# Optimization experiments

Hardware: AMD Instinct MI355X
Metric: run time of the kernel (lower is better)

Reference implementation:

```python
import jax, jax.numpy as jnp
import numpy as np

N = 50000      # nodes
E = 800000     # edges
T = 3          # npass
ED = 64        # embedding_dim
NS = 23        # nshifts (arange(0.8, 3.0+1e-5, 0.1))
MD = NS + ED   # message_dim = 87
H = 200        # hidden width (hardcoded in module)
NMOL = 2048    # number of molecules (segments for final scatter)
RD = ED * (T + 1)  # readout input dim = 256
EPS = 1e-5

SHIFTS = jnp.asarray(np.arange(0.8, 3.0 + 1e-5, 0.1, dtype=np.float32))  # [23]


def setup_inputs() -> dict:
    key = jax.random.key(0)
    ks = jax.random.split(key, 32)
    inp = {
        'z_i': jax.random.randint(ks[0], (N,), 0, 10),
        'edge_index': jax.random.randint(ks[1], (2, E), 0, N),
        'dist_ij': jax.random.uniform(ks[2], (E, 1), dtype=jnp.float32) * 2.2 + 0.8,
        'mol_ind': jnp.sort(jax.random.randint(ks[3], (N,), 0, NMOL)),
        'emb': jax.random.normal(ks[4], (10, ED), dtype=jnp.float32),
        # per-pass update MLP params, stacked over T
        'up_bn_g': jnp.ones((T, MD), jnp.float32),
        'up_bn_b': jnp.zeros((T, MD), jnp.float32),
        'up_w1': jax.random.normal(ks[5], (T, MD, H), jnp.float32) * 0.05,
        'up_b1': jnp.zeros((T, H), jnp.float32),
        'up_w2': jax.random.normal(ks[6], (T, H, H), jnp.float32) * 0.05,
        'up_b2': jnp.zeros((T, H), jnp.float32),
        'up_w3': jax.random.normal(ks[7], (T, H, H), jnp.float32) * 0.05,
        'up_b3': jnp.zeros((T, H), jnp.float32),
        'up_w4': jax.random.normal(ks[8], (T, H, ED), jnp.float32) * 0.05,
        'up_b4': jnp.zeros((T, ED), jnp.float32),
        # readout MLP params
        'ro_bn_g': jnp.ones((RD,), jnp.float32),
        'ro_bn_b': jnp.zeros((RD,), jnp.float32),
        'ro_w1': jax.random.normal(ks[9], (RD, H), jnp.float32) * 0.05,
        'ro_b1': jnp.zeros((H,), jnp.float32),
        'ro_w2': jax.random.normal(ks[10], (H, H), jnp.float32) * 0.05,
        'ro_b2': jnp.zeros((H,), jnp.float32),
        'ro_w3': jax.random.normal(ks[11], (H, H), jnp.float32) * 0.05,
        'ro_b3': jnp.zeros((H,), jnp.float32),
        'ro_w4': jax.random.normal(ks[12], (H, 1), jnp.float32) * 0.05,
        'ro_b4': jnp.zeros((1,), jnp.float32),  # bias filled to 0 in __init__
    }
    return inp


def batchnorm(x, g, b):
    # BatchNorm1d in training mode: batch statistics, biased variance
    mu = jnp.mean(x, axis=0)
    var = jnp.mean(jnp.square(x - mu), axis=0)
    return (x - mu) * jax.lax.rsqrt(var + EPS) * g + b


def mlp(x, g, b, w1, b1, w2, b2, w3, b3, w4, b4):
    x = batchnorm(x, g, b)
    x = jax.nn.relu(x @ w1 + b1)
    x = jax.nn.relu(x @ w2 + b2)
    x = jax.nn.relu(x @ w3 + b3)
    return x @ w4 + b4


def reference(z_i, edge_index, dist_ij, mol_ind, emb,
              up_bn_g, up_bn_b, up_w1, up_b1, up_w2, up_b2, up_w3, up_b3, up_w4, up_b4,
              ro_bn_g, ro_bn_b, ro_w1, ro_b1, ro_w2, ro_b2, ro_w3, ro_b3, ro_w4, ro_b4):
    e_source, e_sink = edge_index[0], edge_index[1]
    rbf_ij = jnp.exp(-jnp.square(dist_ij - SHIFTS[None, :]))  # [E, NS]
    x_i = emb[z_i]                                            # [N, ED]
    x_list = [x_i]
    for t in range(T):
        m_ij = jnp.concatenate([rbf_ij, x_i[e_sink]], axis=1)  # [E, MD] gather
        m_i = jax.ops.segment_sum(m_ij, e_source, num_segments=N)  # scatter-sum
        x_i = x_i + 0.1 * mlp(m_i, up_bn_g[t], up_bn_b[t],
                              up_w1[t], up_b1[t], up_w2[t], up_b2[t],
                              up_w3[t], up_b3[t], up_w4[t], up_b4[t])
        x_list.append(x_i)
    x_all = jnp.concatenate(x_list, axis=1)  # [N, RD]
    y_i = mlp(x_all, ro_bn_g, ro_bn_b, ro_w1, ro_b1, ro_w2, ro_b2, ro_w3, ro_b3, ro_w4, ro_b4)
    y = jax.ops.segment_sum(y_i, mol_ind, num_segments=NMOL)  # [NMOL, 1]
    return y
```

## Files before the change

kernel.cpp:

```cpp
#include <hip/hip_runtime.h>
#include <hip/hip_bf16.h>
#include <type_traits>

#define NN 50000
#define NP 50048
#define EE 800000
#define TT 3
#define ED 64
#define NS 23
#define MD 87
#define HH 200
#define NMOL 2048
#define RD 256

#define SW 232
#define NPB2 512
#define SNB ((NN + 255) / 256)

typedef __attribute__((ext_vector_type(8))) short short8b;
typedef __attribute__((ext_vector_type(4))) float f32x4;

template <int V> using ic = std::integral_constant<int, V>;

__device__ __forceinline__ unsigned short f2bf(float f) {
  unsigned u = __float_as_uint(f);
  return (unsigned short)((u + 0x7fffu + ((u >> 16) & 1u)) >> 16);
}
__device__ __forceinline__ float ubf2f(unsigned short h) {
  return __uint_as_float(((unsigned)h) << 16);
}
__device__ __forceinline__ float bfp2f(unsigned p) {
  return __uint_as_float(p << 16) + __uint_as_float(p & 0xffff0000u);
}
__device__ __forceinline__ unsigned packsplit(float v) {
  unsigned short h = f2bf(v);
  unsigned short l = f2bf(v - ubf2f(h));
  return (unsigned)h | ((unsigned)l << 16);
}

__device__ __forceinline__ void gl2lds16(const short* g, short* l) {
  __builtin_amdgcn_global_load_lds(
      (const __attribute__((address_space(1))) unsigned int*)g,
      (__attribute__((address_space(3))) unsigned int*)l, 16, 0, 0);
}

struct WD { const float* src; short* dst; int K, N, Kpad, Npad, T; };
struct WDs { WD d[5]; };

__global__ __launch_bounds__(256) void wprep_kernel(WDs W) {
  WD w = W.d[blockIdx.y];
  int KB = w.Kpad >> 5, NT = w.Npad >> 4;
  int per = w.Npad * w.Kpad;
  int total = w.T * per;
  for (int idx = blockIdx.x * 256 + threadIdx.x; idx < total; idx += gridDim.x * 256) {
    int t = idx / per;
    int r = idx - t * per;
    int e = r & 7, lane = (r >> 3) & 63;
    int blk = r >> 9;
    int kb = blk % KB, tile = blk / KB;
    int ln = lane & 15, quad = lane >> 4;
    int n = tile * 16 + ln, k = kb * 32 + quad * 8 + e;
    float v = 0.f;
    if (k < w.K && n < w.N) v = w.src[((size_t)t * w.K + k) * w.N + n];
    unsigned short h = f2bf(v);
    unsigned short l = f2bf(v - ubf2f(h));
    size_t base = ((size_t)(t * NT + tile) * KB + kb) * 1024;
    w.dst[base + lane * 8 + e] = (short)h;
    w.dst[base + 512 + lane * 8 + e] = (short)l;
  }
}

__global__ __launch_bounds__(256) void wscale_kernel(const float* __restrict__ wsrc,
                                                     const float* __restrict__ na,
                                                     const float* __restrict__ nb,
                                                     const float* __restrict__ bsrc,
                                                     int K, int Kpad,
                                                     short* __restrict__ wsp,
                                                     float* __restrict__ bc) {
  int n = blockIdx.x;
  int k = threadIdx.x;
  int KB = Kpad >> 5;
  int tile = n >> 4, ln = n & 15;
  float contrib = 0.f;
  if (k < Kpad) {
    float v = 0.f;
    if (n < HH && k < K) {
      float w = wsrc[(size_t)k * HH + n];
      v = na[k] * w;
      contrib = nb[k] * w;
    }
    unsigned short h = f2bf(v);
    unsigned short l = f2bf(v - ubf2f(h));
    int kb = k >> 5, quad = (k & 31) >> 3, e = k & 7;
    int lane = quad * 16 + ln;
    size_t base = ((size_t)tile * KB + kb) * 1024;
    wsp[base + lane * 8 + e] = (short)h;
    wsp[base + 512 + lane * 8 + e] = (short)l;
  }
  __shared__ float sh[256];
  sh[k] = contrib;
  __syncthreads();
  for (int off = 128; off > 0; off >>= 1) {
    if (k < off) sh[k] += sh[k + off];
    __syncthreads();
  }
  if (k == 0) bc[n] = (n < HH ? bsrc[n] : 0.f) + sh[0];
}

__global__ __launch_bounds__(256) void emb_kernel(const int* __restrict__ z,
                                                  const float* __restrict__ emb,
                                                  unsigned* __restrict__ xp,
                                                  short* __restrict__ xq,
                                                  short* __restrict__ xqs) {
  int idx = blockIdx.x * 256 + threadIdx.x;
  if (idx >= NN * ED) return;
  int i = idx >> 6, d = idx & 63;
  unsigned pk = packsplit(emb[z[i] * ED + d]);
  xp[(size_t)i * RD + d] = pk;
  short h = (short)(pk & 0xffffu);
  xq[(size_t)i * RD + d] = h;
  xqs[(size_t)i * ED + d] = h;
}

__global__ __launch_bounds__(256) void hist_kernel(const int* __restrict__ src,
                                                   int* __restrict__ deg) {
  int e = blockIdx.x * 256 + threadIdx.x;
  if (e < EE) atomicAdd(&deg[src[e]], 1);
}

__global__ __launch_bounds__(256) void scanA_kernel(const int* __restrict__ deg,
                                                    int* __restrict__ Psum) {
  int i = blockIdx.x * 256 + threadIdx.x;
  int v = (i < NN) ? deg[i] : 0;
#pragma unroll
  for (int off = 32; off > 0; off >>= 1) v += __shfl_down(v, off, 64);
  __shared__ int ws[4];
  if ((threadIdx.x & 63) == 0) ws[threadIdx.x >> 6] = v;
  __syncthreads();
  if (threadIdx.x == 0) Psum[blockIdx.x] = ws[0] + ws[1] + ws[2] + ws[3];
}

__global__ __launch_bounds__(256) void scanB_kernel(const int* __restrict__ Psum,
                                                    int* __restrict__ Poff) {
  __shared__ int sh[256];
  int t = threadIdx.x;
  int v = (t < SNB) ? Psum[t] : 0;
  sh[t] = v;
  __syncthreads();
  for (int off = 1; off < 256; off <<= 1) {
    int u = (t >= off) ? sh[t - off] : 0;
    __syncthreads();
    sh[t] += u;
    __syncthreads();
  }
  if (t < SNB) Poff[t] = sh[t] - v;
}

__global__ __launch_bounds__(256) void scanC_kernel(const int* __restrict__ deg,
                                                    const int* __restrict__ Poff,
                                                    int* __restrict__ offs,
                                                    int* __restrict__ cursor) {
  __shared__ int sh[256];
  int t = threadIdx.x;
  int i = blockIdx.x * 256 + t;
  int v = (i < NN) ? deg[i] : 0;
  sh[t] = v;
  __syncthreads();
  for (int off = 1; off < 256; off <<= 1) {
    int u = (t >= off) ? sh[t - off] : 0;
    __syncthreads();
    sh[t] += u;
    __syncthreads();
  }
  int excl = Poff[blockIdx.x] + sh[t] - v;
  if (i < NN) {
    offs[i] = excl;
    cursor[i] = excl;
    if (i == NN - 1) offs[NN] = excl + v;
  }
}

__global__ __launch_bounds__(256) void scatter_kernel(const int* __restrict__ src,
                                                      const int* __restrict__ snk,
                                                      const float* __restrict__ dist,
                                                      int* __restrict__ cursor,
                                                      int* __restrict__ ssink,
                                                      float* __restrict__ sdist) {
  int e = blockIdx.x * 256 + threadIdx.x;
  if (e >= EE) return;
  int p = atomicAdd(&cursor[src[e]], 1);
  ssink[p] = snk[e];
  sdist[p] = dist[e];
}

template <bool RBF>
__global__ __launch_bounds__(256) void gather_kernel(const int* __restrict__ offs,
                                                     const int* __restrict__ ssink,
                                                     const float* __restrict__ sdist,
                                                     const short* __restrict__ xqs,
                                                     short* __restrict__ mh) {
  int node = blockIdx.x * 4 + (threadIdx.x >> 6);
  int lane = threadIdx.x & 63;
  if (node >= NN) return;
  float shift = (float)(0.8 + 0.1 * (double)lane);
  int e0 = offs[node], e1 = offs[node + 1];
  float ax0 = 0.f, ax1 = 0.f, ar0 = 0.f, ar1 = 0.f;
  int j = e0;
  for (; j + 4 <= e1; j += 4) {
    int s0 = ssink[j], s1 = ssink[j + 1], s2 = ssink[j + 2], s3 = ssink[j + 3];
    float x0 = ubf2f((unsigned short)xqs[(size_t)s0 * ED + lane]);
    float x1 = ubf2f((unsigned short)xqs[(size_t)s1 * ED + lane]);
    float x2 = ubf2f((unsigned short)xqs[(size_t)s2 * ED + lane]);
    float x3 = ubf2f((unsigned short)xqs[(size_t)s3 * ED + lane]);
    ax0 += x0 + x2;
    ax1 += x1 + x3;
    if (RBF && lane < NS) {
      float d0 = sdist[j], d1 = sdist[j + 1], d2 = sdist[j + 2], d3 = sdist[j + 3];
      float u0 = d0 - shift, u1 = d1 - shift, u2 = d2 - shift, u3 = d3 - shift;
      ar0 += __expf(-u0 * u0) + __expf(-u2 * u2);
      ar1 += __expf(-u1 * u1) + __expf(-u3 * u3);
    }
  }
  for (; j < e1; j++) {
    int s = ssink[j];
    ax0 += ubf2f((unsigned short)xqs[(size_t)s * ED + lane]);
    if (RBF && lane < NS) {
      float u = sdist[j] - shift;
      ar0 += __expf(-u * u);
    }
  }
  float accx = ax0 + ax1;
  if (RBF && lane < NS) mh[(size_t)node * 96 + lane] = (short)f2bf(ar0 + ar1);
  if (RBF && lane >= NS && lane < 32) mh[(size_t)node * 96 + 64 + lane] = 0;
  mh[(size_t)node * 96 + NS + lane] = (short)f2bf(accx);
}

template <int LD>
__global__ __launch_bounds__(256) void colstats_s16_kernel(const short* __restrict__ X,
                                                           float* __restrict__ P) {
  constexpr int CG = LD / 8;
  constexpr int RPB = 256 / CG;
  const int t = threadIdx.x;
  const int cg = t % CG, rin = t / CG;
  float s[8] = {0, 0, 0, 0, 0, 0, 0, 0}, q[8] = {0, 0, 0, 0, 0, 0, 0, 0};
  if (rin < RPB) {
    for (int r = blockIdx.x * RPB + rin; r < NN; r += gridDim.x * RPB) {
      union { uint4 v; short e[8]; } u;
      u.v = *(const uint4*)(X + (size_t)r * LD + cg * 8);
#pragma unroll
      for (int e = 0; e < 8; e++) {
        float f = ubf2f((unsigned short)u.e[e]);
        s[e] += f;
        q[e] += f * f;
      }
    }
  }
  __shared__ float sh[256][16];
#pragma unroll
  for (int e = 0; e < 8; e++) { sh[t][e] = s[e]; sh[t][8 + e] = q[e]; }
  __syncthreads();
  if (rin == 0) {
    for (int rr = 1; rr < RPB; rr++) {
      const float* o = sh[rr * CG + cg];
#pragma unroll
      for (int e = 0; e < 8; e++) { s[e] += o[e]; q[e] += o[8 + e]; }
    }
    float* Pb = P + blockIdx.x * 512;
#pragma unroll
    for (int e = 0; e < 8; e++) {
      Pb[cg * 8 + e] = s[e];
      Pb[256 + cg * 8 + e] = q[e];
    }
  }
}

__global__ __launch_bounds__(256) void bnfinal2_kernel(const float* __restrict__ P, int nblk,
                                                       const float* __restrict__ g,
                                                       const float* __restrict__ b, int ncols,
                                                       float* __restrict__ na,
                                                       float* __restrict__ nb) {
  int c = blockIdx.x;
  int t = threadIdx.x;
  float s = 0.f, q = 0.f;
  for (int i = t; i < nblk; i += 256) {
    s += P[i * 512 + c];
    q += P[i * 512 + 256 + c];
  }
#pragma unroll
  for (int off = 32; off > 0; off >>= 1) {
    s += __shfl_down(s, off, 64);
    q += __shfl_down(q, off, 64);
  }
  __shared__ float ws[4], wq[4];
  if ((t & 63) == 0) { ws[t >> 6] = s; wq[t >> 6] = q; }
  __syncthreads();
  if (t == 0) {
    s = ws[0] + ws[1] + ws[2] + ws[3];
    q = wq[0] + wq[1] + wq[2] + wq[3];
    if (c < ncols) {
      float mean = s / (float)NN;
      float var = q / (float)NN - mean * mean;
      float a = g[c] * rsqrtf(var + 1e-5f);
      na[c] = a;
      nb[c] = b[c] - mean * a;
    } else {
      na[c] = 0.f;
      nb[c] = 0.f;
    }
  }
}

template <bool READOUT>
__global__ __launch_bounds__(256, 2) void fused_kernel(
    const short* __restrict__ Agh,
    const short* __restrict__ W1p, const short* __restrict__ W2p,
    const short* __restrict__ W3p, const short* __restrict__ W4p,
    const float* __restrict__ b1, const float* __restrict__ b2,
    const float* __restrict__ b3, const float* __restrict__ b4,
    unsigned* __restrict__ xp, short* __restrict__ xq, short* __restrict__ xqs,
    int t, const float* __restrict__ w4ro, const int* __restrict__ mol,
    float* __restrict__ out) {
  __shared__ short ldsA[4 * 16 * SW];
  __shared__ short ldsB[2][13 * 512];
  constexpr int GLDA = READOUT ? RD : 96;
  constexpr int KB1 = READOUT ? 8 : 3;
  const int tid = threadIdx.x;
  const int wave = tid >> 6, lane = tid & 63, ln = lane & 15, quad = lane >> 4;
  const int q8 = quad * 8;
  const int bm = blockIdx.x * 64 + wave * 16;
  short* ldsW = ldsA + wave * (16 * SW);
  const short* aRow = ldsW + ln * SW;

#pragma unroll
  for (int p = 0; p < 6; p++) {
    int idx = p * 64 + lane;
    ldsW[(idx / 24) * SW + 208 + (idx % 24)] = 0;
  }

  f32x4 acc[13];
  short8b a[7];

  auto stage = [&](auto ntt, auto kbt, const short* __restrict__ Wp, int s, int buf) {
    constexpr int NT = decltype(ntt)::value;
    constexpr int KB = decltype(kbt)::value;
    const int kb = (s < KB) ? s : s - KB;
    const int plane = (s < KB) ? 0 : 512;
    for (int tile = wave; tile < NT; tile += 4)
      gl2lds16(Wp + (size_t)(tile * KB + kb) * 1024 + plane + lane * 8,
               ldsB[buf] + tile * 512);
  };

  auto runlayer = [&](auto ntt, auto kbt, auto tt, const short8b* af,
                      const short* __restrict__ Wp) {
    constexpr int NT = decltype(ntt)::value;
    constexpr int KB = decltype(kbt)::value;
    constexpr int TERMS = decltype(tt)::value;
    constexpr int NSL = KB * TERMS;
#pragma unroll
    for (int j = 0; j < NT; j++) acc[j] = (f32x4){0.f, 0.f, 0.f, 0.f};
    stage(ntt, kbt, Wp, 0, 0);
    __syncthreads();
#pragma unroll
    for (int s = 0; s < NSL; s++) {
      if (s + 1 < NSL) stage(ntt, kbt, Wp, s + 1, (s + 1) & 1);
      const int kb = (s < KB) ? s : s - KB;
      short8b bh[NT];
#pragma unroll
      for (int j = 0; j < NT; j++)
        bh[j] = *(const short8b*)(ldsB[s & 1] + j * 512 + lane * 8);
#pragma unroll
      for (int j = 0; j < NT; j++)
        acc[j] = __builtin_amdgcn_mfma_f32_16x16x32_bf16(af[kb], bh[j], acc[j], 0, 0, 0);
      __syncthreads();
    }
  };

  auto epi = [&](auto ntt, const float* __restrict__ bias) {
    constexpr int NT = decltype(ntt)::value;
#pragma unroll
    for (int j = 0; j < NT; j++) {
      int colg = j * 16 + ln;
      float bb = (colg < HH) ? bias[colg] : 0.f;
#pragma unroll
      for (int r = 0; r < 4; r++)
        ldsW[(quad * 4 + r) * SW + colg] = (short)f2bf(fmaxf(acc[j][r] + bb, 0.f));
    }
  };
  auto loadA = [&]() {
#pragma unroll
    for (int kb = 0; kb < 7; kb++)
      a[kb] = *(const short8b*)(aRow + kb * 32 + q8);
  };

  {
    short8b a1[KB1];
#pragma unroll
    for (int kb = 0; kb < KB1; kb++)
      a1[kb] = *(const short8b*)(Agh + (size_t)(bm + ln) * GLDA + kb * 32 + q8);
    runlayer(ic<13>{}, ic<KB1>{}, ic<2>{}, a1, W1p);
    epi(ic<13>{}, b1);
  }

  loadA();
  runlayer(ic<13>{}, ic<7>{}, ic<1>{}, a, W2p);
  epi(ic<13>{}, b2);

  loadA();
  runlayer(ic<13>{}, ic<7>{}, ic<1>{}, a, W3p);
  epi(ic<13>{}, b3);

  loadA();

  if constexpr (!READOUT) {
    runlayer(ic<4>{}, ic<7>{}, ic<2>{}, a, W4p);
#pragma unroll
    for (int j = 0; j < 4; j++) {
      int colg = j * 16 + ln;
      float bb = b4[colg];
#pragma unroll
      for (int r = 0; r < 4; r++) {
        int grow = bm + quad * 4 + r;
        if (grow < NN) {
          size_t base = (size_t)grow * RD;
          float oldv = bfp2f(xp[base + (size_t)t * ED + colg]);
          unsigned pk = packsplit(oldv + 0.1f * (acc[j][r] + bb));
          xp[base + (size_t)(t + 1) * ED + colg] = pk;
          short h = (short)(pk & 0xffffu);
          xq[base + (size_t)(t + 1) * ED + colg] = h;
          xqs[(size_t)(t + 1) * NN * ED + (size_t)grow * ED + colg] = h;
        }
      }
    }
  } else {
    float s = 0.f;
#pragma unroll
    for (int kb = 0; kb < 7; kb++)
      if (kb * 32 + q8 < HH)
#pragma unroll
        for (int e = 0; e < 8; e++)
          s += ubf2f((unsigned short)a[kb][e]) * w4ro[kb * 32 + q8 + e];
    s += __shfl_xor(s, 16, 64);
    s += __shfl_xor(s, 32, 64);
    int grow = bm + ln;
    if (lane < 16 && grow < NN) atomicAdd(&out[mol[grow]], s + b4[0]);
  }
}

extern "C" void kernel_launch(void* const* d_in, const int* in_sizes, int n_in,
                              void* d_out, int out_size, void* d_ws, size_t ws_size,
                              hipStream_t stream) {
  const int* z_i = (const int*)d_in[0];
  const int* e_src = (const int*)d_in[1];
  const int* e_snk = ((const int*)d_in[1]) + EE;
  const float* dist = (const float*)d_in[2];
  const int* mol = (const int*)d_in[3];
  const float* emb = (const float*)d_in[4];
  const float* up_bn_g = (const float*)d_in[5];
  const float* up_bn_b = (const float*)d_in[6];
  const float* up_w1 = (const float*)d_in[7];
  const float* up_b1 = (const float*)d_in[8];
  const float* up_w2 = (const float*)d_in[9];
  const float* up_b2 = (const float*)d_in[10];
  const float* up_w3 = (const float*)d_in[11];
  const float* up_b3 = (const float*)d_in[12];
  const float* up_w4 = (const float*)d_in[13];
  const float* up_b4 = (const float*)d_in[14];
  const float* ro_bn_g = (const float*)d_in[15];
  const float* ro_bn_b = (const float*)d_in[16];
  const float* ro_w1 = (const float*)d_in[17];
  const float* ro_b1 = (const float*)d_in[18];
  const float* ro_w2 = (const float*)d_in[19];
  const float* ro_b2 = (const float*)d_in[20];
  const float* ro_w3 = (const float*)d_in[21];
  const float* ro_b3 = (const float*)d_in[22];
  const float* ro_w4 = (const float*)d_in[23];
  const float* ro_b4 = (const float*)d_in[24];
  float* out = (float*)d_out;

  char* p = (char*)d_ws;
  auto alloc = [&](size_t bytes) {
    void* r = (void*)p;
    p += (bytes + 255) & ~(size_t)255;
    return r;
  };
  unsigned* x_p = (unsigned*)alloc((size_t)NN * RD * 4);
  short* x_q = (short*)alloc((size_t)NP * RD * 2);
  short* x_qs = (short*)alloc((size_t)(TT + 1) * NN * ED * 2);
  short* mh = (short*)alloc((size_t)NP * 96 * 2);
  int* ssink = (int*)alloc((size_t)EE * 4);
  float* sdist = (float*)alloc((size_t)EE * 4);
  int* offs = (int*)alloc((size_t)(NN + 1) * 4);
  int* deg = (int*)alloc((size_t)NN * 4);
  int* cursor = (int*)alloc((size_t)NN * 4);
  int* Psum = (int*)alloc((size_t)SNB * 4);
  int* Poff = (int*)alloc((size_t)SNB * 4);
  float* P = (float*)alloc((size_t)NPB2 * 512 * 4);
  float* na = (float*)alloc(256 * 4);
  float* nb = (float*)alloc(256 * 4);
  float* b1c = (float*)alloc(208 * 4);
  short* w1sp = (short*)alloc((size_t)13 * 3 * 1024 * 2);
  short* r1sp = (short*)alloc((size_t)13 * 8 * 1024 * 2);
  short* w2p = (short*)alloc((size_t)TT * 13 * 7 * 1024 * 2);
  short* w3p = (short*)alloc((size_t)TT * 13 * 7 * 1024 * 2);
  short* w4p = (short*)alloc((size_t)TT * 4 * 7 * 1024 * 2);
  short* r2p = (short*)alloc((size_t)13 * 7 * 1024 * 2);
  short* r3p = (short*)alloc((size_t)13 * 7 * 1024 * 2);

  hipMemsetAsync(deg, 0, (size_t)NN * 4, stream);
  hipMemsetAsync(out, 0, (size_t)NMOL * 4, stream);

  WDs descs;
  descs.d[0] = {up_w2, w2p, HH, HH, 224, 208, TT};
  descs.d[1] = {up_w3, w3p, HH, HH, 224, 208, TT};
  descs.d[2] = {up_w4, w4p, HH, ED, 224, 64, TT};
  descs.d[3] = {ro_w2, r2p, HH, HH, 224, 208, 1};
  descs.d[4] = {ro_w3, r3p, HH, HH, 224, 208, 1};
  wprep_kernel<<<dim3(546, 5), 256, 0, stream>>>(descs);

  emb_kernel<<<(NN * ED + 255) / 256, 256, 0, stream>>>(z_i, emb, x_p, x_q, x_qs);
  hist_kernel<<<(EE + 255) / 256, 256, 0, stream>>>(e_src, deg);
  scanA_kernel<<<SNB, 256, 0, stream>>>(deg, Psum);
  scanB_kernel<<<1, 256, 0, stream>>>(Psum, Poff);
  scanC_kernel<<<SNB, 256, 0, stream>>>(deg, Poff, offs, cursor);
  scatter_kernel<<<(EE + 255) / 256, 256, 0, stream>>>(e_src, e_snk, dist, cursor, ssink, sdist);

  const int gM = NP / 64;

  for (int t = 0; t < TT; t++) {
    if (t == 0)
      gather_kernel<true><<<(NN + 3) / 4, 256, 0, stream>>>(
          offs, ssink, sdist, x_qs, mh);
    else
      gather_kernel<false><<<(NN + 3) / 4, 256, 0, stream>>>(
          offs, ssink, sdist, x_qs + (size_t)t * NN * ED, mh);
    colstats_s16_kernel<96><<<NPB2, 256, 0, stream>>>(mh, P);
    bnfinal2_kernel<<<256, 256, 0, stream>>>(P, NPB2, up_bn_g + t * MD, up_bn_b + t * MD, MD,
                                             na, nb);
    wscale_kernel<<<208, 256, 0, stream>>>(up_w1 + (size_t)t * MD * HH, na, nb,
                                           up_b1 + t * HH, MD, 96, w1sp, b1c);
    fused_kernel<false><<<gM, 256, 0, stream>>>(
        mh, w1sp,
        w2p + (size_t)t * 13 * 7 * 1024, w3p + (size_t)t * 13 * 7 * 1024,
        w4p + (size_t)t * 4 * 7 * 1024,
        b1c, up_b2 + t * HH, up_b3 + t * HH, up_b4 + t * ED,
        x_p, x_q, x_qs, t, nullptr, nullptr, nullptr);
  }

  colstats_s16_kernel<256><<<NPB2, 256, 0, stream>>>(x_q, P);
  bnfinal2_kernel<<<256, 256, 0, stream>>>(P, NPB2, ro_bn_g, ro_bn_b, RD, na, nb);
  wscale_kernel<<<208, 256, 0, stream>>>(ro_w1, na, nb, ro_b1, RD, 256, r1sp, b1c);
  fused_kernel<true><<<gM, 256, 0, stream>>>(
      x_q, r1sp, r2p, r3p, nullptr,
      b1c, ro_b2, ro_b3, ro_b4,
      nullptr, nullptr, nullptr, 0, ro_w4, mol, out);

  (void)in_sizes; (void)n_in; (void)out_size; (void)ws_size;
}
```

Baseline: 622.6 us.

## Split MLP output tiles across waves and triple-buffer weight staging with vmcnt waits

The fused MLP kernel previously had each wave own 16 rows and compute all 13 output tiles, so every wave read every weight tile from LDS. Now the 64-row activation block is shared in LDS, and each wave computes 4 row-tiles by a subset of column tiles. This reuses each B fragment across 4 MFMAs and cuts LDS weight reads per wave. Weight staging moves from double to triple buffering with explicit vmcnt waits and raw barriers, prefetching two stages ahead and overlapping the next layer's first loads with the epilogue. In exchange, the activation stride widens, more LDS is used (which may affect occupancy), and the load balance is uneven because 13 tiles split unevenly across 4 waves.

```diff
diff --git a/kernel.cpp b/kernel.cpp
--- a/kernel.cpp
+++ b/kernel.cpp
@@ -13,7 +13,7 @@
 #define NMOL 2048
 #define RD 256
 
-#define SW 232
+#define SW 264
 #define NPB2 512
 #define SNB ((NN + 255) / 256)
 
@@ -42,6 +42,16 @@
   __builtin_amdgcn_global_load_lds(
       (const __attribute__((address_space(1))) unsigned int*)g,
       (__attribute__((address_space(3))) unsigned int*)l, 16, 0, 0);
+}
+
+__device__ __forceinline__ void vmwait(int n) {
+  switch (n) {
+    case 0: asm volatile("s_waitcnt vmcnt(0)" ::: "memory"); break;
+    case 1: asm volatile("s_waitcnt vmcnt(1)" ::: "memory"); break;
+    case 2: asm volatile("s_waitcnt vmcnt(2)" ::: "memory"); break;
+    case 3: asm volatile("s_waitcnt vmcnt(3)" ::: "memory"); break;
+    default: asm volatile("s_waitcnt vmcnt(4)" ::: "memory"); break;
+  }
 }
 
 struct WD { const float* src; short* dst; int K, N, Kpad, Npad, T; };
@@ -320,129 +330,174 @@
     unsigned* __restrict__ xp, short* __restrict__ xq, short* __restrict__ xqs,
     int t, const float* __restrict__ w4ro, const int* __restrict__ mol,
     float* __restrict__ out) {
-  __shared__ short ldsA[4 * 16 * SW];
-  __shared__ short ldsB[2][13 * 512];
+  __shared__ short act[64 * SW];
+  __shared__ short bufW[3][13 * 512];
   constexpr int GLDA = READOUT ? RD : 96;
   constexpr int KB1 = READOUT ? 8 : 3;
   const int tid = threadIdx.x;
   const int wave = tid >> 6, lane = tid & 63, ln = lane & 15, quad = lane >> 4;
   const int q8 = quad * 8;
-  const int bm = blockIdx.x * 64 + wave * 16;
-  short* ldsW = ldsA + wave * (16 * SW);
-  const short* aRow = ldsW + ln * SW;
-
-#pragma unroll
-  for (int p = 0; p < 6; p++) {
-    int idx = p * 64 + lane;
-    ldsW[(idx / 24) * SW + 208 + (idx % 24)] = 0;
-  }
-
-  f32x4 acc[13];
-  short8b a[7];
-
-  auto stage = [&](auto ntt, auto kbt, const short* __restrict__ Wp, int s, int buf) {
-    constexpr int NT = decltype(ntt)::value;
-    constexpr int KB = decltype(kbt)::value;
-    const int kb = (s < KB) ? s : s - KB;
-    const int plane = (s < KB) ? 0 : 512;
-    for (int tile = wave; tile < NT; tile += 4)
-      gl2lds16(Wp + (size_t)(tile * KB + kb) * 1024 + plane + lane * 8,
-               ldsB[buf] + tile * 512);
+  const int bm = blockIdx.x * 64;
+
+  if constexpr (!READOUT) {
+#pragma unroll
+    for (int i = 0; i < 3; i++) {
+      int idx = tid + 256 * i;
+      int row = idx / 12, col = (idx - row * 12) * 8;
+      *(uint4*)(act + row * SW + col) =
+          *(const uint4*)(Agh + (size_t)(bm + row) * GLDA + col);
+    }
+    {
+      int row = tid >> 2, c = 208 + (tid & 3) * 4;
+      *(uint2*)(act + row * SW + c) = (uint2){0u, 0u};
+    }
+  } else {
+#pragma unroll
+    for (int i = 0; i < 8; i++) {
+      int idx = tid + 256 * i;
+      int row = idx >> 5, col = (idx & 31) * 8;
+      *(uint4*)(act + row * SW + col) =
+          *(const uint4*)(Agh + (size_t)(bm + row) * GLDA + col);
+    }
+  }
+  __syncthreads();
+
+  f32x4 acc[4][4];
+  short8b a[4];
+
+  auto stage = [&](const short* __restrict__ Wp, int NT, int KB, int TERMS,
+                   int s, int bi) {
+    int kb = (TERMS == 2) ? (s >> 1) : s;
+    int pl = (TERMS == 2) ? ((s & 1) << 9) : 0;
+    short* dst = &bufW[bi][0];
+#pragma unroll
+    for (int j = 0; j < 4; j++) {
+      int tile = wave + 4 * j;
+      if (tile < NT)
+        gl2lds16(Wp + (size_t)(tile * KB + kb) * 1024 + pl + lane * 8,
+                 dst + tile * 512);
+    }
   };
 
-  auto runlayer = [&](auto ntt, auto kbt, auto tt, const short8b* af,
-                      const short* __restrict__ Wp) {
+  auto runloop = [&](auto ntt, auto kbt, auto tt, const short* __restrict__ Wp) {
     constexpr int NT = decltype(ntt)::value;
     constexpr int KB = decltype(kbt)::value;
     constexpr int TERMS = decltype(tt)::value;
     constexpr int NSL = KB * TERMS;
-#pragma unroll
-    for (int j = 0; j < NT; j++) acc[j] = (f32x4){0.f, 0.f, 0.f, 0.f};
-    stage(ntt, kbt, Wp, 0, 0);
-    __syncthreads();
+    constexpr int NJ = (NT + 3) >> 2;
+    const int ntw = (NT - wave + 3) >> 2;
+#pragma unroll
+    for (int j = 0; j < NJ; j++)
+#pragma unroll
+      for (int i = 0; i < 4; i++) acc[j][i] = (f32x4){0.f, 0.f, 0.f, 0.f};
 #pragma unroll
     for (int s = 0; s < NSL; s++) {
-      if (s + 1 < NSL) stage(ntt, kbt, Wp, s + 1, (s + 1) & 1);
-      const int kb = (s < KB) ? s : s - KB;
-      short8b bh[NT];
-#pragma unroll
-      for (int j = 0; j < NT; j++)
-        bh[j] = *(const short8b*)(ldsB[s & 1] + j * 512 + lane * 8);
-#pragma unroll
-      for (int j = 0; j < NT; j++)
-        acc[j] = __builtin_amdgcn_mfma_f32_16x16x32_bf16(af[kb], bh[j], acc[j], 0, 0, 0);
-      __syncthreads();
+      vmwait((s < NSL - 1) ? ntw : 0);
+      __builtin_amdgcn_s_barrier();
+      __builtin_amdgcn_sched_barrier(0);
+      if (s + 2 < NSL) stage(Wp, NT, KB, TERMS, s + 2, (s + 2) % 3);
+      if (TERMS == 1 || (s & 1) == 0) {
+        const int kb = (TERMS == 2) ? (s >> 1) : s;
+#pragma unroll
+        for (int i = 0; i < 4; i++)
+          a[i] = *(const short8b*)(act + (i * 16 + ln) * SW + kb * 32 + q8);
+      }
+      const short* bw = &bufW[s % 3][0];
+#pragma unroll
+      for (int j = 0; j < NJ; j++) {
+        int tile = wave + 4 * j;
+        if (tile < NT) {
+          short8b b = *(const short8b*)(bw + tile * 512 + lane * 8);
+#pragma unroll
+          for (int i = 0; i < 4; i++)
+            acc[j][i] =
+                __builtin_amdgcn_mfma_f32_16x16x32_bf16(a[i], b, acc[j][i], 0, 0, 0);
+        }
+      }
     }
   };
 
   auto epi = [&](auto ntt, const float* __restrict__ bias) {
     constexpr int NT = decltype(ntt)::value;
-#pragma unroll
-    for (int j = 0; j < NT; j++) {
-      int colg = j * 16 + ln;
-      float bb = (colg < HH) ? bias[colg] : 0.f;
-#pragma unroll
-      for (int r = 0; r < 4; r++)
-        ldsW[(quad * 4 + r) * SW + colg] = (short)f2bf(fmaxf(acc[j][r] + bb, 0.f));
+    constexpr int NJ = (NT + 3) >> 2;
+#pragma unroll
+    for (int j = 0; j < NJ; j++) {
+      int tile = wave + 4 * j;
+      if (tile < NT) {
+        int colg = tile * 16 + ln;
+        float bb = (colg < HH) ? bias[colg] : 0.f;
+#pragma unroll
+        for (int i = 0; i < 4; i++)
+#pragma unroll
+          for (int r = 0; r < 4; r++)
+            act[(i * 16 + quad * 4 + r) * SW + colg] =
+                (short)f2bf(fmaxf(acc[j][i][r] + bb, 0.f));
+      }
     }
   };
-  auto loadA = [&]() {
-#pragma unroll
-    for (int kb = 0; kb < 7; kb++)
-      a[kb] = *(const short8b*)(aRow + kb * 32 + q8);
+
+  auto lgkmbar = [&]() {
+    asm volatile("s_waitcnt lgkmcnt(0)" ::: "memory");
+    __builtin_amdgcn_s_barrier();
+    __builtin_amdgcn_sched_barrier(0);
   };
 
-  {
-    short8b a1[KB1];
-#pragma unroll
-    for (int kb = 0; kb < KB1; kb++)
-      a1[kb] = *(const short8b*)(Agh + (size_t)(bm + ln) * GLDA + kb * 32 + q8);
-    runlayer(ic<13>{}, ic<KB1>{}, ic<2>{}, a1, W1p);
-    epi(ic<13>{}, b1);
-  }
-
-  loadA();
-  runlayer(ic<13>{}, ic<7>{}, ic<1>{}, a, W2p);
+  stage(W1p, 13, KB1, 2, 0, 0);
+  stage(W1p, 13, KB1, 2, 1, 1);
+  runloop(ic<13>{}, ic<KB1>{}, ic<2>{}, W1p);
+  __builtin_amdgcn_s_barrier();
+  __builtin_amdgcn_sched_barrier(0);
+  stage(W2p, 13, 7, 1, 0, 0);
+  stage(W2p, 13, 7, 1, 1, 1);
+  epi(ic<13>{}, b1);
+  lgkmbar();
+
+  runloop(ic<13>{}, ic<7>{}, ic<1>{}, W2p);
+  __builtin_amdgcn_s_barrier();
+  __builtin_amdgcn_sched_barrier(0);
+  stage(W3p, 13, 7, 1, 0, 0);
+  stage(W3p, 13, 7, 1, 1, 1);
   epi(ic<13>{}, b2);
-
-  loadA();
-  runlayer(ic<13>{}, ic<7>{}, ic<1>{}, a, W3p);
-  epi(ic<13>{}, b3);
-
-  loadA();
+  lgkmbar();
+
+  runloop(ic<13>{}, ic<7>{}, ic<1>{}, W3p);
+  __builtin_amdgcn_s_barrier();
+  __builtin_amdgcn_sched_barrier(0);
 
   if constexpr (!READOUT) {
-    runlayer(ic<4>{}, ic<7>{}, ic<2>{}, a, W4p);
-#pragma unroll
-    for (int j = 0; j < 4; j++) {
-      int colg = j * 16 + ln;
-      float bb = b4[colg];
+    stage(W4p, 4, 7, 2, 0, 0);
+    stage(W4p, 4, 7, 2, 1, 1);
+    epi(ic<13>{}, b3);
+    lgkmbar();
+    runloop(ic<4>{}, ic<7>{}, ic<2>{}, W4p);
+    int colg = wave * 16 + ln;
+    float bb = b4[colg];
+#pragma unroll
+    for (int i = 0; i < 4; i++)
 #pragma unroll
       for (int r = 0; r < 4; r++) {
-        int grow = bm + quad * 4 + r;
+        int grow = bm + i * 16 + quad * 4 + r;
         if (grow < NN) {
           size_t base = (size_t)grow * RD;
           float oldv = bfp2f(xp[base + (size_t)t * ED + colg]);
-          unsigned pk = packsplit(oldv + 0.1f * (acc[j][r] + bb));
+          unsigned pk = packsplit(oldv + 0.1f * (acc[0][i][r] + bb));
           xp[base + (size_t)(t + 1) * ED + colg] = pk;
           short h = (short)(pk & 0xffffu);
           xq[base + (size_t)(t + 1) * ED + colg] = h;
           xqs[(size_t)(t + 1) * NN * ED + (size_t)grow * ED + colg] = h;
         }
       }
-    }
   } else {
+    epi(ic<13>{}, b3);
+    lgkmbar();
+    int row = tid >> 2;
     float s = 0.f;
-#pragma unroll
-    for (int kb = 0; kb < 7; kb++)
-      if (kb * 32 + q8 < HH)
-#pragma unroll
-        for (int e = 0; e < 8; e++)
-          s += ubf2f((unsigned short)a[kb][e]) * w4ro[kb * 32 + q8 + e];
-    s += __shfl_xor(s, 16, 64);
-    s += __shfl_xor(s, 32, 64);
-    int grow = bm + ln;
-    if (lane < 16 && grow < NN) atomicAdd(&out[mol[grow]], s + b4[0]);
+    for (int c = (tid & 3); c < HH; c += 4)
+      s += ubf2f((unsigned short)act[row * SW + c]) * w4ro[c];
+    s += __shfl_xor(s, 1, 64);
+    s += __shfl_xor(s, 2, 64);
+    int grow = bm + row;
+    if ((tid & 3) == 0 && grow < NN) atomicAdd(&out[mol[grow]], s + b4[0]);
   }
 }
 
```

After: 612.7 us. No clear change (-1.6%).
